# Kernel tuning notes

Measured on AMD Instinct MI355X. Metric: run time of the kernel, lower is better.

Reference implementation:

```python
import jax, jax.numpy as jnp
import numpy as np

MASK_VALUE = 0.0
LEAKY_SLOPE = 0.2  # tf.keras 'leaky_relu' activation default negative_slope

B, T, F, H, OUT = 256, 512, 256, 1024, 64


def setup_inputs() -> dict:
    key = jax.random.key(0)
    ks = jax.random.split(key, 5)
    x = jax.random.normal(ks[0], (B, T, F), dtype=jnp.float32)
    W = jax.random.normal(ks[1], (F, 4 * H), dtype=jnp.float32) * 0.05
    U = jax.random.normal(ks[2], (H, 4 * H), dtype=jnp.float32) * 0.05
    b = jnp.zeros((4 * H,), dtype=jnp.float32)
    W1 = jax.random.normal(ks[3], (3 * H, H), dtype=jnp.float32) * 0.02
    b1 = jnp.zeros((H,), dtype=jnp.float32)
    W2 = jax.random.normal(ks[4], (H, OUT), dtype=jnp.float32) * 0.02
    b2 = jnp.zeros((OUT,), dtype=jnp.float32)
    return {"x": x, "W": W, "U": U, "b": b, "W1": W1, "b1": b1, "W2": W2, "b2": b2}


def _lstm_final_state(x, mask, W, U, b):
    """Masked LSTM (Keras gate order i,f,g,o); masked steps carry state through.
    Returns final (h, c), each [B, H]. Dropout layers are identity at inference."""
    h0 = jnp.zeros((x.shape[0], H), dtype=x.dtype)
    c0 = jnp.zeros((x.shape[0], H), dtype=x.dtype)
    # Precompute input projection for all timesteps in one big GEMM: [B,T,4H]
    xz = jnp.einsum('btf,fg->btg', x, W) + b

    def step(carry, inp):
        h, c = carry
        xz_t, m_t = inp  # [B,4H], [B]
        z = xz_t + h @ U
        i, f, g, o = jnp.split(z, 4, axis=-1)
        i = jax.nn.sigmoid(i)
        f = jax.nn.sigmoid(f)
        g = jnp.tanh(g)
        o = jax.nn.sigmoid(o)
        c_new = f * c + i * g
        h_new = o * jnp.tanh(c_new)
        m = m_t[:, None]
        h = jnp.where(m, h_new, h)
        c = jnp.where(m, c_new, c)
        return (h, c), None

    xs = (jnp.swapaxes(xz, 0, 1), jnp.swapaxes(mask, 0, 1))  # time-major
    (h, c), _ = jax.lax.scan(step, (h0, c0), xs)
    return h, c


def reference(x, W, U, b, W1, b1, W2, b2):
    mask = jnp.any(x != MASK_VALUE, axis=2)  # [B,T]
    h, c = _lstm_final_state(x, mask, W, U, b)
    # return_state=True with return_sequences=False -> (out, h, c), out == h
    feat = jnp.concatenate([h, h, c], axis=1)  # [B, 3H]
    y = jax.nn.leaky_relu(feat @ W1 + b1, negative_slope=LEAKY_SLOPE)
    return y @ W2 + b2
```

## Files before the change

kernel.cpp:

```cpp
#include <hip/hip_runtime.h>

#define Tt_ 512
#define Ff_ 256
#define Hh_ 1024

typedef unsigned short u16;
typedef unsigned long long u64;
typedef __attribute__((ext_vector_type(8))) short bf16x8;
typedef __attribute__((ext_vector_type(4))) float f32x4;
typedef __attribute__((ext_vector_type(2))) unsigned int u32x2;

#define MFMA(a, b, c) __builtin_amdgcn_mfma_f32_16x16x32_bf16(a, b, c, 0, 0, 0)

__device__ __forceinline__ float bf2f(u16 u){
  union { unsigned int i; float f; } v; v.i = ((unsigned int)u) << 16; return v.f;
}
__device__ __forceinline__ u16 f2bf(float f){
  union { float f; unsigned int i; } v; v.f = f;
  return (u16)((v.i + 0x7FFFu + ((v.i >> 16) & 1u)) >> 16);
}
__device__ __forceinline__ float sigm(float z){ return 1.0f / (1.0f + __expf(-z)); }
__device__ __forceinline__ float tanh_(float z){ return 1.0f - 2.0f / (__expf(2.0f * z) + 1.0f); }
__device__ __forceinline__ float getE(const void* p, size_t i, int isf32){
  return isf32 ? ((const float*)p)[i] : bf2f(((const u16*)p)[i]);
}

template<int SEL>
__device__ __forceinline__ float qb(float v, int lbase){
#if __has_builtin(__builtin_amdgcn_mov_dpp)
  int r = __builtin_amdgcn_mov_dpp(__builtin_bit_cast(int, v), SEL * 0x55, 0xF, 0xF, true);
  return __builtin_bit_cast(float, r);
#else
  return __shfl(v, lbase + SEL, 64);
#endif
}

__global__ void detect_dtype(const u16* __restrict__ p, int* __restrict__ flag){
  int tid = threadIdx.x;
  int plausible = 0;
  for (int i = tid; i < 4096; i += 256){
    u16 u = p[2 * i];
    int ex = (u >> 7) & 0xFF;
    plausible += (((u & 0x7FFF) == 0) || (ex >= 87 && ex <= 133)) ? 1 : 0;
  }
  __shared__ int red[256];
  red[tid] = plausible; __syncthreads();
  for (int s = 128; s > 0; s >>= 1){ if (tid < s) red[tid] += red[tid + s]; __syncthreads(); }
  if (tid == 0) *flag = (red[0] < (4096 * 3) / 5) ? 1 : 0;
}

__global__ void convert_x(const void* __restrict__ x, u16* __restrict__ xb, const int* __restrict__ flags){
  size_t i = ((size_t)blockIdx.x * 256 + threadIdx.x) * 8;
  if (flags[0]){
    const float* xf = (const float*)x + i;
    u16 o[8];
    #pragma unroll
    for (int j = 0; j < 8; ++j) o[j] = f2bf(xf[j]);
    *(bf16x8*)(xb + i) = *(const bf16x8*)o;
  } else {
    *(bf16x8*)(xb + i) = *(const bf16x8*)((const u16*)x + i);
  }
}

__global__ void pack_wu(const void* __restrict__ W, const void* __restrict__ U,
                        const int* __restrict__ flags, u16* __restrict__ WUp){
  int fW = flags[1], fU = flags[2];
  int u = blockIdx.x * 256 + threadIdx.x;
  int nt = u / 10240;
  int rem = u - nt * 10240;
  int kg = rem >> 6, c64 = rem & 63;
  int pc = nt * 64 + c64;
  int g = pc & 3;
  int gb = ((g & 1) << 1) | (g >> 1);
  int oc = gb * 1024 + (pc >> 2);
  u16* dst = WUp + (size_t)u * 8;
  #pragma unroll
  for (int j = 0; j < 8; ++j){
    int k = kg * 8 + j;
    float v = (k < 256) ? getE(W, (size_t)k * 4096 + oc, fW)
                        : getE(U, (size_t)(k - 256) * 4096 + oc, fU);
    dst[j] = f2bf(v);
  }
}

__global__ void pack_w1(const void* __restrict__ W1, const int* __restrict__ flags, u16* __restrict__ W1p){
  int f1 = flags[3];
  int u = blockIdx.x * 256 + threadIdx.x;
  int nt = u >> 14;
  int kg = (u >> 6) & 255, c64 = u & 63;
  int n = nt * 64 + c64;
  u16* dst = W1p + (size_t)u * 8;
  #pragma unroll
  for (int j = 0; j < 8; ++j){
    int k = kg * 8 + j;
    float a = (k < 1024) ? getE(W1, (size_t)k * 1024 + n, f1) : 0.0f;
    a += getE(W1, (size_t)(k + 1024) * 1024 + n, f1);
    dst[j] = f2bf(a);
  }
}

__global__ void pack_w2(const void* __restrict__ W2, const int* __restrict__ flags, u16* __restrict__ W2p){
  int f2 = flags[4];
  int u = blockIdx.x * 256 + threadIdx.x;
  int kg = u >> 6, c64 = u & 63;
  u16* dst = W2p + (size_t)u * 8;
  #pragma unroll
  for (int j = 0; j < 8; ++j) dst[j] = f2bf(getE(W2, (size_t)(kg * 8 + j) * 64 + c64, f2));
}

__global__ void pack_bias(const u16* __restrict__ b, float* __restrict__ br){
  int u = blockIdx.x * 256 + threadIdx.x;
  int g = u & 3;
  int gb = ((g & 1) << 1) | (g >> 1);
  br[u] = bf2f(b[gb * 1024 + (u >> 2)]);
}

__global__ void mask_kernel(const u16* __restrict__ xb, unsigned char* __restrict__ mkT){
  int w = threadIdx.x >> 6, lane = threadIdx.x & 63;
  int row = blockIdx.x * 4 + w;
  u32x2 v = *((const u32x2*)(xb + (size_t)row * 256) + lane);
  int nz = (((v.x & 0x7FFF7FFFu) | (v.y & 0x7FFF7FFFu)) != 0u);
  int a = __any(nz);
  if (lane == 0){
    int b = row >> 9, t = row & 511;
    mkT[(size_t)t * 256 + b] = (unsigned char)(a ? 1 : 0);
  }
}

__launch_bounds__(512, 1)
__global__ void lstm_step(const u16* __restrict__ x, const u16* __restrict__ WUp,
                          const float* __restrict__ br, const unsigned char* __restrict__ mkT,
                          u16* __restrict__ hb0, u16* __restrict__ hb1,
                          u16* __restrict__ cfin, unsigned int* flg32){
  __shared__ u64 hsm[8192];
  __shared__ u16 hstg[1024];
  __shared__ u16 Bc[2][22528];
  const int tid = threadIdx.x, bid = blockIdx.x;
  const int lane = tid & 63, w = tid >> 6;
  const int quad = lane >> 4, l15 = lane & 15;
  const int g  = (bid >> 3) & 7;
  const int c  = (bid & 7) | ((bid >> 6) << 3);
  const int r0 = g * 32;
  const int tile = w >> 2;
  const int nt = c * 2 + tile;
  const int bc0 = (w & 3) * 16 + l15;
  const u16* Bb = WUp + (size_t)nt * 81920;
  const int pc0 = c * 128 + w * 16 + l15;
  const float bias0 = br[pc0];
  const int slot = lane & 3, lbase = lane & 60;
  const int jl0 = w * 4 + (l15 >> 2);
  const int rowE = quad * 4;
  const size_t xrowA = (size_t)(r0 + l15) * (Tt_ * Ff_);
  const size_t xrowB = xrowA + (size_t)16 * Tt_ * Ff_;
  const int swzA = (l15 & 7) << 4;
  char* hb = (char*)hsm;
  const unsigned int* fpA = flg32 + (((g << 5) + (lane & 15)) << 4);
  const unsigned int* fpB = fpA + (16 << 4);
  unsigned int* myflag = flg32 + (((g << 5) + c) << 4);
  const int hr   = tid >> 4;
  const int hc16 = tid & 15;
  const size_t hgoff = (size_t)(r0 + hr) * Hh_ + hc16 * 4;
  const int hldsb = hr * 2048;
  const int hswz = (hr & 7) << 4;
  const int hcb = hc16 * 8;

  for (int i = tid; i < 5632; i += 512){
    int tl = i / 2816, rem = i - tl * 2816;
    *(bf16x8*)&Bc[tl][rem * 8] =
      *(const bf16x8*)(WUp + (size_t)(c * 2 + tl) * 81920 + (size_t)rem * 8);
  }
  __syncthreads();

  f32x4 cst[2];
  { f32x4 z4 = {0.f, 0.f, 0.f, 0.f}; cst[0] = z4; cst[1] = z4; }

  f32x4 accx[2];
  { f32x4 i0 = {bias0, bias0, bias0, bias0}; accx[0] = i0; accx[1] = i0; }
  {
    const u16* xp = x;
    #pragma unroll
    for (int ks = 0; ks < 8; ++ks){
      int kq = ks * 32 + quad * 8;
      bf16x8 a0 = *(const bf16x8*)(xp + xrowA + kq);
      bf16x8 a1 = *(const bf16x8*)(xp + xrowB + kq);
      bf16x8 b0 = *(const bf16x8*)(&Bc[tile][ks * 2048 + quad * 512 + bc0 * 8]);
      accx[0] = MFMA(a0, b0, accx[0]);
      accx[1] = MFMA(a1, b0, accx[1]);
    }
  }

  for (int t = 0; t < Tt_; ++t){
    const u16* hin  = (t & 1) ? hb1 : hb0;
    u16*       hout = (t & 1) ? hb0 : hb1;
    const unsigned int tgt = (unsigned int)t;

    while (__ballot(__hip_atomic_load(fpA, __ATOMIC_RELAXED, __HIP_MEMORY_SCOPE_AGENT) >= tgt)
           != ~0ull){}
    asm volatile("" ::: "memory");
    u64 hA[8], hB[8];
    #pragma unroll
    for (int i = 0; i < 8; ++i)
      hA[i] = __hip_atomic_load((const u64*)(hin + hgoff + i * 64),
                                __ATOMIC_RELAXED, __HIP_MEMORY_SCOPE_AGENT);

    while (__ballot(__hip_atomic_load(fpB, __ATOMIC_RELAXED, __HIP_MEMORY_SCOPE_AGENT) >= tgt)
           != ~0ull){}
    asm volatile("" ::: "memory");
    #pragma unroll
    for (int i = 0; i < 8; ++i)
      hB[i] = __hip_atomic_load((const u64*)(hin + hgoff + (i + 8) * 64),
                                __ATOMIC_RELAXED, __HIP_MEMORY_SCOPE_AGENT);

    unsigned int mka = *(const unsigned int*)(mkT + (size_t)t * 256 + r0 + rowE);
    unsigned int mkb = *(const unsigned int*)(mkT + (size_t)t * 256 + r0 + rowE + 16);

    f32x4 acc[2];
    acc[0] = accx[0]; acc[1] = accx[1];

    #pragma unroll
    for (int i = 0; i < 8; ++i)
      *(u64*)(hb + hldsb + ((i * 128 + hcb) ^ hswz)) = hA[i];
    __syncthreads();

    #pragma unroll
    for (int ks = 0; ks < 3; ++ks){
      int cb = ks * 64 + quad * 16;
      bf16x8 a0 = *(const bf16x8*)(hb + l15 * 2048 + (cb ^ swzA));
      bf16x8 a1 = *(const bf16x8*)(hb + (l15 + 16) * 2048 + (cb ^ swzA));
      bf16x8 b0 = *(const bf16x8*)(&Bc[tile][(ks + 8) * 2048 + quad * 512 + bc0 * 8]);
      acc[0] = MFMA(a0, b0, acc[0]);
      acc[1] = MFMA(a1, b0, acc[1]);
    }
    #pragma unroll
    for (int ks = 3; ks < 16; ++ks){
      int cb = ks * 64 + quad * 16;
      bf16x8 a0 = *(const bf16x8*)(hb + l15 * 2048 + (cb ^ swzA));
      bf16x8 a1 = *(const bf16x8*)(hb + (l15 + 16) * 2048 + (cb ^ swzA));
      bf16x8 b0 = *(const bf16x8*)(Bb + (size_t)((ks + 8) * 4 + quad) * 512 + bc0 * 8);
      acc[0] = MFMA(a0, b0, acc[0]);
      acc[1] = MFMA(a1, b0, acc[1]);
    }

    #pragma unroll
    for (int i = 0; i < 8; ++i)
      *(u64*)(hb + hldsb + (((i + 8) * 128 + hcb) ^ hswz)) = hB[i];
    __syncthreads();

    #pragma unroll
    for (int ks = 16; ks < 32; ++ks){
      int cb = ks * 64 + quad * 16;
      bf16x8 a0 = *(const bf16x8*)(hb + l15 * 2048 + (cb ^ swzA));
      bf16x8 a1 = *(const bf16x8*)(hb + (l15 + 16) * 2048 + (cb ^ swzA));
      bf16x8 b0 = *(const bf16x8*)(Bb + (size_t)((ks + 8) * 4 + quad) * 512 + bc0 * 8);
      acc[0] = MFMA(a0, b0, acc[0]);
      acc[1] = MFMA(a1, b0, acc[1]);
    }

    #pragma unroll
    for (int mf = 0; mf < 2; ++mf){
      unsigned int mk4 = mf ? mkb : mka;
      #pragma unroll
      for (int reg = 0; reg < 4; ++reg){
        float z = acc[mf][reg];
        float v = (slot == 1) ? tanh_(z) : sigm(z);
        float vi = qb<0>(v, lbase);
        float vg = qb<1>(v, lbase);
        float vf = qb<2>(v, lbase);
        float vo = qb<3>(v, lbase);
        float cv = cst[mf][reg];
        float cn = fmaf(vf, cv, vi * vg);
        float hn = vo * tanh_(cn);
        if (!((mk4 >> (8 * reg)) & 1u)){
          cn = cv;
          int rl = rowE + reg + mf * 16;
          int jh = c * 32 + jl0;
          hn = bf2f(*(const u16*)(hb + rl * 2048 + ((jh * 2) ^ ((rl & 7) << 4))));
        }
        cst[mf][reg] = cn;
        if (slot == 0){
          int rl = rowE + reg + mf * 16;
          hstg[rl * 32 + jl0] = f2bf(hn);
        }
      }
    }
    __syncthreads();

    if (tid < 256){
      u64 val = ((const u64*)hstg)[tid];
      __hip_atomic_store((u64*)(hout + (size_t)(r0 + (tid >> 3)) * Hh_ + c * 32 + (tid & 7) * 4),
                         val, __ATOMIC_RELAXED, __HIP_MEMORY_SCOPE_AGENT);
    }
    __syncthreads();

    if (tid == 0)
      __hip_atomic_store(myflag, (unsigned int)(t + 1),
                         __ATOMIC_RELAXED, __HIP_MEMORY_SCOPE_AGENT);

    if (t < Tt_ - 1){
      { f32x4 i0 = {bias0, bias0, bias0, bias0}; accx[0] = i0; accx[1] = i0; }
      const u16* xp = x + (size_t)(t + 1) * Ff_;
      #pragma unroll
      for (int ks = 0; ks < 8; ++ks){
        int kq = ks * 32 + quad * 8;
        bf16x8 a0 = *(const bf16x8*)(xp + xrowA + kq);
        bf16x8 a1 = *(const bf16x8*)(xp + xrowB + kq);
        bf16x8 b0 = *(const bf16x8*)(&Bc[tile][ks * 2048 + quad * 512 + bc0 * 8]);
        accx[0] = MFMA(a0, b0, accx[0]);
        accx[1] = MFMA(a1, b0, accx[1]);
      }
    }
  }

  #pragma unroll
  for (int mf = 0; mf < 2; ++mf)
    #pragma unroll
    for (int reg = 0; reg < 4; ++reg)
      if (slot == 0){
        int r = r0 + rowE + reg + mf * 16;
        cfin[(size_t)r * Hh_ + c * 32 + jl0] = f2bf(cst[mf][reg]);
      }
}

__launch_bounds__(256, 1)
__global__ void gemm_head(const u16* __restrict__ A1, const u16* __restrict__ A2,
                          int kSplit, int kSlices, const u16* __restrict__ Bp,
                          int Ntiles, const u16* __restrict__ bias, int act,
                          void* __restrict__ outp, int ldOut, int outF32){
  const int tid = threadIdx.x, bid = blockIdx.x;
  const int lane = tid & 63, w = tid >> 6;
  const int wm = w >> 1, wn = w & 1;
  const int quad = lane >> 4, l15 = lane & 15;
  const int mt = bid / Ntiles, nt = bid - mt * Ntiles;
  const int r0 = mt * 64 + wm * 32 + l15;
  const size_t arow0 = (size_t)r0 * 1024;
  const size_t arow1 = arow0 + (size_t)16 * 1024;
  const int bc0 = wn * 32 + l15;
  const u16* Bb = Bp + (size_t)nt * kSlices * 2048;
  f32x4 acc[2][2];
  { f32x4 z4 = {0.f, 0.f, 0.f, 0.f}; acc[0][0] = z4; acc[0][1] = z4; acc[1][0] = z4; acc[1][1] = z4; }
  #pragma unroll 4
  for (int ks = 0; ks < kSlices; ++ks){
    const u16* ap; int kq;
    if (ks < kSplit){ ap = A1; kq = ks * 32 + quad * 8; }
    else            { ap = A2; kq = (ks - kSplit) * 32 + quad * 8; }
    bf16x8 a0 = *(const bf16x8*)(ap + arow0 + kq);
    bf16x8 a1 = *(const bf16x8*)(ap + arow1 + kq);
    const u16* bp = Bb + (size_t)(ks * 4 + quad) * 512;
    bf16x8 b0 = *(const bf16x8*)(bp + bc0 * 8);
    bf16x8 b1 = *(const bf16x8*)(bp + bc0 * 8 + 128);
    acc[0][0] = MFMA(a0, b0, acc[0][0]);
    acc[0][1] = MFMA(a0, b1, acc[0][1]);
    acc[1][0] = MFMA(a1, b0, acc[1][0]);
    acc[1][1] = MFMA(a1, b1, acc[1][1]);
  }
  #pragma unroll
  for (int mf = 0; mf < 2; ++mf)
    #pragma unroll
    for (int nf = 0; nf < 2; ++nf){
      int cB = nt * 64 + bc0 + nf * 16;
      #pragma unroll
      for (int reg = 0; reg < 4; ++reg){
        int r = mt * 64 + wm * 32 + mf * 16 + quad * 4 + reg;
        float zv = acc[mf][nf][reg] + bf2f(bias[cB]);
        if (act) zv = (zv > 0.f) ? zv : 0.2f * zv;
        if (outF32) ((float*)outp)[(size_t)r * ldOut + cB] = zv;
        else        ((u16*)outp)[(size_t)r * ldOut + cB] = f2bf(zv);
      }
    }
}

extern "C" void kernel_launch(void* const* d_in, const int* in_sizes, int n_in,
                              void* d_out, int out_size, void* d_ws, size_t ws_size,
                              hipStream_t stream){
  const void* x  = d_in[0];
  const void* W  = d_in[1];
  const void* U  = d_in[2];
  const u16*  b  = (const u16*)d_in[3];
  const void* W1 = d_in[4];
  const u16*  b1 = (const u16*)d_in[5];
  const void* W2 = d_in[6];
  const u16*  b2 = (const u16*)d_in[7];
  char* ws = (char*)d_ws;
  size_t o = 0;
  u16* WUp = (u16*)(ws + o);            o += 10485760;
  u16* W1p = (u16*)(ws + o);            o += 4194304;
  u16* W2p = (u16*)(ws + o);            o += 131072;
  float* br = (float*)(ws + o);         o += 16384;
  unsigned char* mk = (unsigned char*)(ws + o); o += 131072;
  u16* hb0 = (u16*)(ws + o);            o += 524288;
  u16* hb1 = (u16*)(ws + o);            o += 524288;
  u16* cfin = (u16*)(ws + o);           o += 524288;
  u16* yb  = (u16*)(ws + o);            o += 524288;
  unsigned int* flg32 = (unsigned int*)(ws + o); o += 16384;
  int* flg = (int*)(ws + o);            o += 512;
  u16* xb  = (u16*)(ws + o);            o += 67108864;
  if (ws_size < o) return;

  hipMemsetAsync(hb0, 0, 524288, stream);
  hipMemsetAsync(flg32, 0, 16384, stream);
  detect_dtype<<<1, 256, 0, stream>>>((const u16*)x,  flg + 0);
  detect_dtype<<<1, 256, 0, stream>>>((const u16*)W,  flg + 1);
  detect_dtype<<<1, 256, 0, stream>>>((const u16*)U,  flg + 2);
  detect_dtype<<<1, 256, 0, stream>>>((const u16*)W1, flg + 3);
  detect_dtype<<<1, 256, 0, stream>>>((const u16*)W2, flg + 4);
  convert_x<<<16384, 256, 0, stream>>>(x, xb, flg);
  pack_wu<<<2560, 256, 0, stream>>>(W, U, flg, WUp);
  pack_w1<<<1024, 256, 0, stream>>>(W1, flg, W1p);
  pack_w2<<<32, 256, 0, stream>>>(W2, flg, W2p);
  pack_bias<<<16, 256, 0, stream>>>(b, br);
  mask_kernel<<<32768, 256, 0, stream>>>(xb, mk);
  lstm_step<<<256, 512, 0, stream>>>(xb, WUp, br, mk, hb0, hb1, cfin, flg32);
  gemm_head<<<64, 256, 0, stream>>>(hb0, cfin, 32, 64, W1p, 16, b1, 1, yb, 1024, 0);
  gemm_head<<<4, 256, 0, stream>>>(yb, yb, 32, 32, W2p, 1, b2, 0, d_out, 64, 1);
}
```

Baseline: 5.119 ms.

## Replace per-block step flags with per-wave counter barrier and double-buffered LDS

The per-block completion flags are replaced by eight shared per-wave atomic counters per row group. Each wave publishes its slice of h directly and increments its counter, so the two block-wide barriers around the h store are gone and consumers do a single poll for 32 arrivals. The LDS h buffer is double-buffered so the next step can start without a trailing sync. The LDS weight cache is dropped: the x-projection weights and the next step's x operands are held in registers, and the x MFMAs move into the step itself. Launch bounds are raised to two blocks per CU, which caps registers and risks spilling, and the x-projection work now sits on the per-step critical path.

```diff
diff --git a/kernel.cpp b/kernel.cpp
--- a/kernel.cpp
+++ b/kernel.cpp
@@ -127,14 +127,13 @@
   }
 }
 
-__launch_bounds__(512, 1)
+__launch_bounds__(512, 2)
 __global__ void lstm_step(const u16* __restrict__ x, const u16* __restrict__ WUp,
                           const float* __restrict__ br, const unsigned char* __restrict__ mkT,
                           u16* __restrict__ hb0, u16* __restrict__ hb1,
-                          u16* __restrict__ cfin, unsigned int* flg32){
-  __shared__ u64 hsm[8192];
-  __shared__ u16 hstg[1024];
-  __shared__ u16 Bc[2][22528];
+                          u16* __restrict__ cfin, unsigned int* barW){
+  __shared__ u64 hsm[2][8192];
+  __shared__ u16 hstgW[8][32][4];
   const int tid = threadIdx.x, bid = blockIdx.x;
   const int lane = tid & 63, w = tid >> 6;
   const int quad = lane >> 4, l15 = lane & 15;
@@ -142,9 +141,8 @@
   const int c  = (bid & 7) | ((bid >> 6) << 3);
   const int r0 = g * 32;
   const int tile = w >> 2;
-  const int nt = c * 2 + tile;
   const int bc0 = (w & 3) * 16 + l15;
-  const u16* Bb = WUp + (size_t)nt * 81920;
+  const u16* Bb = WUp + (size_t)(c * 2 + tile) * 81920;
   const int pc0 = c * 128 + w * 16 + l15;
   const float bias0 = br[pc0];
   const int slot = lane & 3, lbase = lane & 60;
@@ -153,10 +151,8 @@
   const size_t xrowA = (size_t)(r0 + l15) * (Tt_ * Ff_);
   const size_t xrowB = xrowA + (size_t)16 * Tt_ * Ff_;
   const int swzA = (l15 & 7) << 4;
-  char* hb = (char*)hsm;
-  const unsigned int* fpA = flg32 + (((g << 5) + (lane & 15)) << 4);
-  const unsigned int* fpB = fpA + (16 << 4);
-  unsigned int* myflag = flg32 + (((g << 5) + c) << 4);
+  const unsigned int* pollp = barW + (((g << 3) + (lane & 7)) << 4);
+  unsigned int* myctr = barW + (((g << 3) + w) << 4);
   const int hr   = tid >> 4;
   const int hc16 = tid & 15;
   const size_t hgoff = (size_t)(r0 + hr) * Hh_ + hc16 * 4;
@@ -164,48 +160,42 @@
   const int hswz = (hr & 7) << 4;
   const int hcb = hc16 * 8;
 
-  for (int i = tid; i < 5632; i += 512){
-    int tl = i / 2816, rem = i - tl * 2816;
-    *(bf16x8*)&Bc[tl][rem * 8] =
-      *(const bf16x8*)(WUp + (size_t)(c * 2 + tl) * 81920 + (size_t)rem * 8);
-  }
-  __syncthreads();
+  bf16x8 bprex[8];
+  #pragma unroll
+  for (int i = 0; i < 8; ++i)
+    bprex[i] = *(const bf16x8*)(Bb + (size_t)(i * 4 + quad) * 512 + bc0 * 8);
+
+  bf16x8 xa[8][2];
+  {
+    const u16* xp = x;
+    #pragma unroll
+    for (int ks = 0; ks < 8; ++ks){
+      int kq = ks * 32 + quad * 8;
+      xa[ks][0] = *(const bf16x8*)(xp + xrowA + kq);
+      xa[ks][1] = *(const bf16x8*)(xp + xrowB + kq);
+    }
+  }
 
   f32x4 cst[2];
   { f32x4 z4 = {0.f, 0.f, 0.f, 0.f}; cst[0] = z4; cst[1] = z4; }
-
-  f32x4 accx[2];
-  { f32x4 i0 = {bias0, bias0, bias0, bias0}; accx[0] = i0; accx[1] = i0; }
-  {
-    const u16* xp = x;
-    #pragma unroll
-    for (int ks = 0; ks < 8; ++ks){
-      int kq = ks * 32 + quad * 8;
-      bf16x8 a0 = *(const bf16x8*)(xp + xrowA + kq);
-      bf16x8 a1 = *(const bf16x8*)(xp + xrowB + kq);
-      bf16x8 b0 = *(const bf16x8*)(&Bc[tile][ks * 2048 + quad * 512 + bc0 * 8]);
-      accx[0] = MFMA(a0, b0, accx[0]);
-      accx[1] = MFMA(a1, b0, accx[1]);
-    }
-  }
 
   for (int t = 0; t < Tt_; ++t){
     const u16* hin  = (t & 1) ? hb1 : hb0;
     u16*       hout = (t & 1) ? hb0 : hb1;
-    const unsigned int tgt = (unsigned int)t;
-
-    while (__ballot(__hip_atomic_load(fpA, __ATOMIC_RELAXED, __HIP_MEMORY_SCOPE_AGENT) >= tgt)
-           != ~0ull){}
+    char* hb = (char*)hsm[t & 1];
+
+    {
+      const unsigned int tgt = 32u * (unsigned int)t;
+      while (__ballot(__hip_atomic_load(pollp, __ATOMIC_RELAXED, __HIP_MEMORY_SCOPE_AGENT) >= tgt)
+             != ~0ull){}
+    }
     asm volatile("" ::: "memory");
+
     u64 hA[8], hB[8];
     #pragma unroll
     for (int i = 0; i < 8; ++i)
       hA[i] = __hip_atomic_load((const u64*)(hin + hgoff + i * 64),
                                 __ATOMIC_RELAXED, __HIP_MEMORY_SCOPE_AGENT);
-
-    while (__ballot(__hip_atomic_load(fpB, __ATOMIC_RELAXED, __HIP_MEMORY_SCOPE_AGENT) >= tgt)
-           != ~0ull){}
-    asm volatile("" ::: "memory");
     #pragma unroll
     for (int i = 0; i < 8; ++i)
       hB[i] = __hip_atomic_load((const u64*)(hin + hgoff + (i + 8) * 64),
@@ -215,7 +205,12 @@
     unsigned int mkb = *(const unsigned int*)(mkT + (size_t)t * 256 + r0 + rowE + 16);
 
     f32x4 acc[2];
-    acc[0] = accx[0]; acc[1] = accx[1];
+    { f32x4 i0 = {bias0, bias0, bias0, bias0}; acc[0] = i0; acc[1] = i0; }
+    #pragma unroll
+    for (int ks = 0; ks < 8; ++ks){
+      acc[0] = MFMA(xa[ks][0], bprex[ks], acc[0]);
+      acc[1] = MFMA(xa[ks][1], bprex[ks], acc[1]);
+    }
 
     #pragma unroll
     for (int i = 0; i < 8; ++i)
@@ -223,16 +218,7 @@
     __syncthreads();
 
     #pragma unroll
-    for (int ks = 0; ks < 3; ++ks){
-      int cb = ks * 64 + quad * 16;
-      bf16x8 a0 = *(const bf16x8*)(hb + l15 * 2048 + (cb ^ swzA));
-      bf16x8 a1 = *(const bf16x8*)(hb + (l15 + 16) * 2048 + (cb ^ swzA));
-      bf16x8 b0 = *(const bf16x8*)(&Bc[tile][(ks + 8) * 2048 + quad * 512 + bc0 * 8]);
-      acc[0] = MFMA(a0, b0, acc[0]);
-      acc[1] = MFMA(a1, b0, acc[1]);
-    }
-    #pragma unroll
-    for (int ks = 3; ks < 16; ++ks){
+    for (int ks = 0; ks < 16; ++ks){
       int cb = ks * 64 + quad * 16;
       bf16x8 a0 = *(const bf16x8*)(hb + l15 * 2048 + (cb ^ swzA));
       bf16x8 a1 = *(const bf16x8*)(hb + (l15 + 16) * 2048 + (cb ^ swzA));
@@ -279,34 +265,28 @@
         cst[mf][reg] = cn;
         if (slot == 0){
           int rl = rowE + reg + mf * 16;
-          hstg[rl * 32 + jl0] = f2bf(hn);
+          hstgW[w][rl][l15 >> 2] = f2bf(hn);
         }
       }
     }
-    __syncthreads();
-
-    if (tid < 256){
-      u64 val = ((const u64*)hstg)[tid];
-      __hip_atomic_store((u64*)(hout + (size_t)(r0 + (tid >> 3)) * Hh_ + c * 32 + (tid & 7) * 4),
+
+    asm volatile("s_waitcnt lgkmcnt(0)" ::: "memory");
+    if (lane < 32){
+      u64 val = *(const u64*)&hstgW[w][lane][0];
+      __hip_atomic_store((u64*)(hout + (size_t)(r0 + lane) * Hh_ + c * 32 + w * 4),
                          val, __ATOMIC_RELAXED, __HIP_MEMORY_SCOPE_AGENT);
     }
-    __syncthreads();
-
-    if (tid == 0)
-      __hip_atomic_store(myflag, (unsigned int)(t + 1),
-                         __ATOMIC_RELAXED, __HIP_MEMORY_SCOPE_AGENT);
+    asm volatile("s_waitcnt vmcnt(0)" ::: "memory");
 
     if (t < Tt_ - 1){
-      { f32x4 i0 = {bias0, bias0, bias0, bias0}; accx[0] = i0; accx[1] = i0; }
+      if (lane == 0)
+        __hip_atomic_fetch_add(myctr, 1u, __ATOMIC_RELAXED, __HIP_MEMORY_SCOPE_AGENT);
       const u16* xp = x + (size_t)(t + 1) * Ff_;
       #pragma unroll
       for (int ks = 0; ks < 8; ++ks){
         int kq = ks * 32 + quad * 8;
-        bf16x8 a0 = *(const bf16x8*)(xp + xrowA + kq);
-        bf16x8 a1 = *(const bf16x8*)(xp + xrowB + kq);
-        bf16x8 b0 = *(const bf16x8*)(&Bc[tile][ks * 2048 + quad * 512 + bc0 * 8]);
-        accx[0] = MFMA(a0, b0, accx[0]);
-        accx[1] = MFMA(a1, b0, accx[1]);
+        xa[ks][0] = *(const bf16x8*)(xp + xrowA + kq);
+        xa[ks][1] = *(const bf16x8*)(xp + xrowB + kq);
       }
     }
   }
@@ -391,13 +371,13 @@
   u16* hb1 = (u16*)(ws + o);            o += 524288;
   u16* cfin = (u16*)(ws + o);           o += 524288;
   u16* yb  = (u16*)(ws + o);            o += 524288;
-  unsigned int* flg32 = (unsigned int*)(ws + o); o += 16384;
+  unsigned int* barW = (unsigned int*)(ws + o); o += 4096;
   int* flg = (int*)(ws + o);            o += 512;
   u16* xb  = (u16*)(ws + o);            o += 67108864;
   if (ws_size < o) return;
 
   hipMemsetAsync(hb0, 0, 524288, stream);
-  hipMemsetAsync(flg32, 0, 16384, stream);
+  hipMemsetAsync(barW, 0, 4096, stream);
   detect_dtype<<<1, 256, 0, stream>>>((const u16*)x,  flg + 0);
   detect_dtype<<<1, 256, 0, stream>>>((const u16*)W,  flg + 1);
   detect_dtype<<<1, 256, 0, stream>>>((const u16*)U,  flg + 2);
@@ -409,7 +389,7 @@
   pack_w2<<<32, 256, 0, stream>>>(W2, flg, W2p);
   pack_bias<<<16, 256, 0, stream>>>(b, br);
   mask_kernel<<<32768, 256, 0, stream>>>(xb, mk);
-  lstm_step<<<256, 512, 0, stream>>>(xb, WUp, br, mk, hb0, hb1, cfin, flg32);
+  lstm_step<<<256, 512, 0, stream>>>(xb, WUp, br, mk, hb0, hb1, cfin, barW);
   gemm_head<<<64, 256, 0, stream>>>(hb0, cfin, 32, 64, W1p, 16, b1, 1, yb, 1024, 0);
   gemm_head<<<4, 256, 0, stream>>>(yb, yb, 32, 32, W2p, 1, b2, 0, d_out, 64, 1);
 }
```

Measured after the change: 13.98 ms. 2.73x slower.
